# Kernel optimization log

Measured on AMD Instinct MI355X. Metric: run time of the kernel, lower is better.

## Reference

```python
import jax, jax.numpy as jnp
import numpy as np

B, N, D = 16, 2048, 1024


def _linear_params(key, d, scale):
    kw, kb = jax.random.split(key)
    W = jax.random.uniform(kw, (d, d), jnp.float32, -scale, scale)
    b = jax.random.uniform(kb, (d,), jnp.float32, -scale, scale)
    return W, b


def setup_inputs() -> dict:
    key = jax.random.key(0)
    ks = jax.random.split(key, 9)
    scale = 1.0 / np.sqrt(D)  # torch nn.Linear default init range
    x1 = jax.random.normal(ks[0], (B, N, D), jnp.float32)
    x2 = jax.random.normal(ks[1], (B, N, D), jnp.float32)
    Wq, bq = _linear_params(ks[2], D, scale)
    Wk, bk = _linear_params(ks[3], D, scale)
    Wv, bv = _linear_params(ks[4], D, scale)
    W1, b1 = _linear_params(ks[5], D, scale)
    W2, b2 = _linear_params(ks[6], D, scale)
    W3, b3 = _linear_params(ks[7], D, scale)
    # torch init is zeros(1); use small nonzero so output/grad paths are exercised
    gamma = jax.random.normal(ks[8], (1,), jnp.float32) * 0.1
    return {"x1": x1, "x2": x2, "Wq": Wq, "bq": bq, "Wk": Wk, "bk": bk,
            "Wv": Wv, "bv": bv, "W1": W1, "b1": b1, "W2": W2, "b2": b2,
            "W3": W3, "b3": b3, "gamma": gamma}


def reference(x1, x2, Wq, bq, Wk, bk, Wv, bv, W1, b1, W2, b2, W3, b3, gamma):
    # QKV cross-attention (unscaled softmax, as in the torch source)
    q = jnp.einsum('bnd,ed->bne', x1, Wq) + bq
    k = jnp.einsum('bnd,ed->bne', x2, Wk) + bk
    v = jnp.einsum('bnd,ed->bne', x2, Wv) + bv
    energy = jnp.einsum('bik,bjk->bij', q, k)          # [B, N, N]
    attn = jax.nn.softmax(energy, axis=-1)
    out = jnp.einsum('bij,bjk->bik', attn, v)          # [B, N, D]
    # multiscale sigmoid gate: sigmoid(s1 + s2 + s3)
    s = (jnp.einsum('bnd,ed->bne', out, W1) + b1
         + jnp.einsum('bnd,ed->bne', out, W2) + b2
         + jnp.einsum('bnd,ed->bne', out, W3) + b3)
    out = out * jax.nn.sigmoid(s)
    return gamma * out + x1
```

## Files before the change

kernel.cpp:

```cpp
#include <hip/hip_runtime.h>
#include <hip/hip_bf16.h>
#include <hip/hip_fp16.h>
#include <cstdint>

#define B_ 16
#define N_ 2048
#define D_ 1024

typedef __attribute__((ext_vector_type(4))) float f32x4;
typedef __attribute__((ext_vector_type(8))) short s16x8;

typedef __attribute__((address_space(1))) const void* gas_ptr;
typedef __attribute__((address_space(3))) void* las_ptr;

__device__ __forceinline__ void gload16(const void* g, void* l)
{
    __builtin_amdgcn_global_load_lds((gas_ptr)(uintptr_t)g, (las_ptr)(uintptr_t)l, 16, 0, 0);
}

__device__ __forceinline__ ushort f2bf(float f)
{
    union { __hip_bfloat16 h; ushort u; } c;
    c.h = __float2bfloat16(f);
    return c.u;
}
__device__ __forceinline__ float bf2f(ushort u)
{
    union { __hip_bfloat16 h; ushort u; } c;
    c.u = u;
    return __bfloat162float(c.h);
}

__global__ __launch_bounds__(256)
void cvt2_bf16(const float* __restrict__ in1, const float* __restrict__ in2,
               ushort* __restrict__ o1, ushort* __restrict__ o2, long n)
{
    long i = ((long)blockIdx.x * 256 + threadIdx.x) * 8;
    const long stride = (long)gridDim.x * 256 * 8;
    for (; i < n; i += stride) {
        f32x4 a = *(const f32x4*)(in1 + i);
        f32x4 b = *(const f32x4*)(in1 + i + 4);
        s16x8 o;
#pragma unroll
        for (int j = 0; j < 4; ++j) { o[j] = (short)f2bf(a[j]); o[4 + j] = (short)f2bf(b[j]); }
        *(s16x8*)(o1 + i) = o;
        f32x4 c = *(const f32x4*)(in2 + i);
        f32x4 d = *(const f32x4*)(in2 + i + 4);
        s16x8 p;
#pragma unroll
        for (int j = 0; j < 4; ++j) { p[j] = (short)f2bf(c[j]); p[4 + j] = (short)f2bf(d[j]); }
        *(s16x8*)(o2 + i) = p;
    }
}

__global__ __launch_bounds__(256)
void prep_w(const float* __restrict__ Wq, const float* __restrict__ Wk, const float* __restrict__ Wv,
            const float* __restrict__ W1, const float* __restrict__ W2, const float* __restrict__ W3,
            const float* __restrict__ b1, const float* __restrict__ b2, const float* __restrict__ b3,
            const float* __restrict__ bq, const float* __restrict__ bk,
            ushort* __restrict__ wq, ushort* __restrict__ wk, ushort* __restrict__ wv,
            ushort* __restrict__ wsum, float* __restrict__ bsum, float* __restrict__ bqk)
{
    const long i = ((long)blockIdx.x * 256 + threadIdx.x) * 4;
    if (i < (long)D_ * D_) {
#pragma unroll
        for (int j = 0; j < 4; ++j) {
            wq[i + j] = f2bf(Wq[i + j]);
            wk[i + j] = f2bf(Wk[i + j]);
            wv[i + j] = f2bf(Wv[i + j]);
            wsum[i + j] = f2bf(W1[i + j] + W2[i + j] + W3[i + j]);
        }
        if (i < D_) {
#pragma unroll
            for (int j = 0; j < 4; ++j) {
                bsum[i + j] = b1[i + j] + b2[i + j] + b3[i + j];
                bqk[i + j] = bq[i + j];
                bqk[D_ + i + j] = bk[i + j];
            }
        }
    }
}

template<int EPI>
__global__ __launch_bounds__(512, 2)
void gemm256(const ushort* __restrict__ A, const ushort* __restrict__ Bw,
             void* __restrict__ Out, const float* __restrict__ bias,
             int Nn, int K, int NT,
             long sA, long sB, long sO, int bstride,
             const ushort* __restrict__ outb, const float* __restrict__ x1r,
             const float* __restrict__ gamma)
{
    __shared__ ushort lds[65536];
    const int tid = threadIdx.x;
    const int l = tid & 63;
    const int w = tid >> 6;
    const int wm = w >> 2, wn = w & 3;
    const int lr = l & 15;
    const int c2x = ((((l >> 4) * 16) ^ ((lr & 8) << 2)) >> 1);

    const int gx = gridDim.x, gy = gridDim.y;
    const int nwg = gx * gy * (int)gridDim.z;
    const int orig = ((int)blockIdx.z * gy + blockIdx.y) * gx + blockIdx.x;
    const int swzb = (orig & 7) * (nwg >> 3) + (orig >> 3);
    const int gxy = gx * gy;
    const int bz = swzb / gxy;
    const int rem = swzb - bz * gxy;
    const int by = rem / gx;
    const int bx = rem - by * gx;
    const int m0 = by * 256, n0 = bx * 256;

    const ushort* Ab = A + (long)bz * sA;
    const ushort* Bb = Bw + (long)bz * sB;

    int srow[2], scol[2];
#pragma unroll
    for (int i = 0; i < 2; ++i) {
        const int L = (i * 512 + tid) * 16;
        const int P = L ^ (((L >> 9) & 1) << 5);
        srow[i] = (P >> 6) & 127;
        scol[i] = ((P >> 13) << 5) | ((P & 63) >> 1);
    }
    const int sdst = w * 512;

    f32x4 acc[8][4];
#pragma unroll
    for (int i = 0; i < 8; ++i)
#pragma unroll
        for (int j = 0; j < 4; ++j) acc[i][j] = f32x4{0.f, 0.f, 0.f, 0.f};
    s16x8 a[4][2], b[2][2][2];

#define STAGEH(pl, t)                                                                     \
    if ((t) < NT) {                                                                       \
        const int rb2 = (t) & 1;                                                          \
        const long kk = (long)(t) << 6;                                                   \
        _Pragma("unroll")                                                                 \
        for (int i = 0; i < 2; ++i) {                                                     \
            if ((pl) < 2)                                                                 \
                gload16(Ab + (long)(m0 + (pl) * 128 + srow[i]) * K + kk + scol[i],        \
                        &lds[rb2 * 16384 + (pl) * 8192 + sdst + i * 4096]);               \
            else                                                                          \
                gload16(Bb + (long)(n0 + ((pl) - 2) * 128 + srow[i]) * K + kk + scol[i],  \
                        &lds[32768 + rb2 * 16384 + ((pl) - 2) * 8192 + sdst + i * 4096]); \
        }                                                                                 \
    }

#define LDA_(qm)                                                                           \
    _Pragma("unroll") for (int mi = 0; mi < 4; ++mi)                                       \
    _Pragma("unroll") for (int ks = 0; ks < 2; ++ks)                                       \
        a[mi][ks] = *(const s16x8*)&lds[rbase_a + ks * 4096 + ((qm) * 64 + mi * 16 + lr) * 32 + c2x];

#define LDB_(qn)                                                                           \
    _Pragma("unroll") for (int ni = 0; ni < 2; ++ni)                                       \
    _Pragma("unroll") for (int ks = 0; ks < 2; ++ks)                                       \
        b[qn][ni][ks] = *(const s16x8*)&lds[rbase_b + ks * 4096 +                          \
            ((wn & 1) * 64 + (qn) * 32 + ni * 16 + lr) * 32 + c2x];

#define MM_(qm, qn)                                                                        \
    __builtin_amdgcn_s_setprio(1);                                                         \
    _Pragma("unroll") for (int mi = 0; mi < 4; ++mi)                                       \
    _Pragma("unroll") for (int ni = 0; ni < 2; ++ni)                                       \
    _Pragma("unroll") for (int ks = 0; ks < 2; ++ks)                                       \
        acc[(qm) * 4 + mi][(qn) * 2 + ni] = __builtin_amdgcn_mfma_f32_16x16x32_bf16(       \
            a[mi][ks], b[qn][ni][ks], acc[(qm) * 4 + mi][(qn) * 2 + ni], 0, 0, 0);         \
    __builtin_amdgcn_s_setprio(0);

#define BARR __builtin_amdgcn_s_barrier()

#define KGROUP(tt, VMSTR) {                                          \
    const int rb = (tt) & 1;                                         \
    const int rbase_a = rb * 16384 + wm * 8192;                      \
    const int rbase_b = 32768 + rb * 16384 + (wn >> 1) * 8192;       \
                                                            \
    LDB_(0); LDA_(0);                                                \
    STAGEH(1, (tt) + 1);                                             \
    BARR; MM_(0, 0); BARR;                                           \
                                                            \
    LDB_(1);                                                         \
    STAGEH(2, (tt) + 1);                                             \
    BARR; MM_(0, 1); BARR;                                           \
                                                            \
    LDA_(1);                                                         \
    STAGEH(3, (tt) + 1);                                             \
    BARR; MM_(1, 0); BARR;                                           \
     \
    MM_(1, 1);                                                       \
    STAGEH(0, (tt) + 2);                                             \
    asm volatile("s_waitcnt " VMSTR ::: "memory");                   \
    BARR; }

    STAGEH(0, 0); STAGEH(1, 0); STAGEH(2, 0); STAGEH(3, 0);
    STAGEH(0, 1);
    asm volatile("s_waitcnt vmcnt(2)" ::: "memory");
    BARR;

    int t = 0;
    for (; t < NT - 2; ++t) KGROUP(t, "vmcnt(2)");
    for (; t < NT; ++t) KGROUP(t, "vmcnt(0)");

#undef KGROUP
#undef STAGEH
#undef LDA_
#undef LDB_
#undef MM_

    float gam = 0.f;
    if (EPI == 3) gam = *gamma;
#pragma unroll
    for (int am = 0; am < 8; ++am) {
#pragma unroll
        for (int an = 0; an < 4; ++an) {
#pragma unroll
            for (int r = 0; r < 4; ++r) {
                const int m = m0 + wm * 128 + am * 16 + (l >> 4) * 4 + r;
                const int n = n0 + wn * 64 + an * 16 + lr;
                const float v = acc[am][an][r];
                const long o = (long)bz * sO + (long)m * Nn + n;
                if (EPI == 0) {
                    ((ushort*)Out)[o] = f2bf(v + bias[bz * bstride + n]);
                } else if (EPI == 1) {
                    union { __half h; ushort u; } c;
                    c.h = __float2half(v);
                    ((ushort*)Out)[o] = c.u;
                } else if (EPI == 2) {
                    ((ushort*)Out)[o] = f2bf(v);
                } else if (EPI == 4) {
                    ((ushort*)Out)[o] = f2bf(v + bias[m]);
                } else {
                    const float s = v + bias[n];
                    const float g = 1.f / (1.f + __expf(-s));
                    const float ov = bf2f(outb[(long)m * Nn + n]);
                    ((float*)Out)[o] = gam * ov * g + x1r[(long)m * Nn + n];
                }
            }
        }
    }
}

__global__ __launch_bounds__(256)
void softmax_inplace(ushort* __restrict__ EA)
{
    const long row = blockIdx.x;
    ushort* p = EA + row * N_;
    const int tid = threadIdx.x;
    const int c0 = tid * 8;
    __shared__ float red[8];

    s16x8 raw = *(const s16x8*)(p + c0);
    float v[8];
    float mx = -3.0e38f;
#pragma unroll
    for (int i = 0; i < 8; ++i) {
        union { ushort u; __half h; } c;
        c.u = (ushort)raw[i];
        v[i] = __half2float(c.h);
        mx = fmaxf(mx, v[i]);
    }
#pragma unroll
    for (int off = 32; off > 0; off >>= 1) mx = fmaxf(mx, __shfl_xor(mx, off));
    if ((tid & 63) == 0) red[tid >> 6] = mx;
    __syncthreads();
    mx = fmaxf(fmaxf(red[0], red[1]), fmaxf(red[2], red[3]));

    float s = 0.f;
#pragma unroll
    for (int i = 0; i < 8; ++i) { v[i] = __expf(v[i] - mx); s += v[i]; }
#pragma unroll
    for (int off = 32; off > 0; off >>= 1) s += __shfl_xor(s, off);
    if ((tid & 63) == 0) red[4 + (tid >> 6)] = s;
    __syncthreads();
    s = (red[4] + red[5]) + (red[6] + red[7]);
    const float inv = 1.f / s;

    s16x8 o;
#pragma unroll
    for (int i = 0; i < 8; ++i) o[i] = (short)f2bf(v[i] * inv);
    *(s16x8*)(p + c0) = o;
}

extern "C" void kernel_launch(void* const* d_in, const int* in_sizes, int n_in,
                              void* d_out, int out_size, void* d_ws, size_t ws_size,
                              hipStream_t stream)
{
    const float* x1 = (const float*)d_in[0];
    const float* x2 = (const float*)d_in[1];
    const float* Wq = (const float*)d_in[2];
    const float* bq = (const float*)d_in[3];
    const float* Wk = (const float*)d_in[4];
    const float* bk = (const float*)d_in[5];
    const float* Wv = (const float*)d_in[6];
    const float* bv = (const float*)d_in[7];
    const float* W1 = (const float*)d_in[8];
    const float* b1 = (const float*)d_in[9];
    const float* W2 = (const float*)d_in[10];
    const float* b2 = (const float*)d_in[11];
    const float* W3 = (const float*)d_in[12];
    const float* b3 = (const float*)d_in[13];
    const float* gamma = (const float*)d_in[14];
    float* out = (float*)d_out;

    char* ws = (char*)d_ws;
    const long SZ_XB = (long)B_ * N_ * D_ * 2;
    ushort* x1b  = (ushort*)(ws);
    ushort* x2b  = (ushort*)(ws + SZ_XB);
    ushort* EA   = (ushort*)(ws);
    ushort* wqb  = (ushort*)(ws + 2 * SZ_XB);
    ushort* wkb  = (ushort*)(ws + 2 * SZ_XB + 1L * 2097152);
    ushort* wvb  = (ushort*)(ws + 2 * SZ_XB + 2L * 2097152);
    ushort* wsb  = (ushort*)(ws + 2 * SZ_XB + 3L * 2097152);
    float*  bsum = (float*) (ws + 2 * SZ_XB + 4L * 2097152);
    float*  bqk  = (float*) (ws + 2 * SZ_XB + 4L * 2097152 + 4096);
    char* base2  = ws + 2 * SZ_XB + 4L * 2097152 + 16384;
    ushort* Qb   = (ushort*)(base2);
    ushort* Kb   = (ushort*)(base2 + SZ_XB);
    ushort* Vtb  = (ushort*)(base2 + 2 * SZ_XB);
    ushort* outb = Kb;

    const long NE = (long)B_ * N_ * D_;

    cvt2_bf16<<<4096, 256, 0, stream>>>(x1, x2, x1b, x2b, NE);
    prep_w<<<1024, 256, 0, stream>>>(Wq, Wk, Wv, W1, W2, W3, b1, b2, b3, bq, bk,
                                     wqb, wkb, wvb, wsb, bsum, bqk);

    gemm256<0><<<dim3(4, 128, 2), 512, 0, stream>>>(x1b, wqb, Qb, bqk,
        D_, D_, 16, NE, (long)D_ * D_, NE, D_, nullptr, nullptr, nullptr);

    gemm256<4><<<dim3(8, 4, 16), 512, 0, stream>>>(wvb, x2b, Vtb, bv,
        N_, D_, 16, 0, (long)N_ * D_, (long)D_ * N_, 0,
        nullptr, nullptr, nullptr);

    gemm256<1><<<dim3(8, 8, 16), 512, 0, stream>>>(Qb, Kb, EA, nullptr,
        N_, D_, 16, (long)N_ * D_, (long)N_ * D_, (long)N_ * N_, 0,
        nullptr, nullptr, nullptr);

    softmax_inplace<<<B_ * N_, 256, 0, stream>>>(EA);

    gemm256<2><<<dim3(4, 8, 16), 512, 0, stream>>>(EA, Vtb, outb, nullptr,
        D_, N_, 32, (long)N_ * N_, (long)D_ * N_, (long)N_ * D_, 0,
        nullptr, nullptr, nullptr);

    gemm256<3><<<dim3(4, 128, 1), 512, 0, stream>>>(outb, wsb, out, bsum,
        D_, D_, 16, 0, 0, 0, 0, outb, x1, gamma);
}
```

Baseline: 730.5 us.

## Replace barrier-interleaved k-loop with ping-pong wave ordering and single barrier

Restructures the GEMM main loop so that even and odd waves run their four MFMA quadrants in opposite orders. All four prefetch stages for the next tile are issued up front, and the three intra-iteration barriers are dropped, leaving one barrier per k-step. Prefetch depth shrinks from a partially two-ahead pipeline to strictly one tile ahead with a full vmcnt(0) wait. The aim is to cut barrier stalls and to stagger LDS and MFMA use across waves, at the cost of less latency hiding for global loads.

```diff
diff --git a/kernel.cpp b/kernel.cpp
--- a/kernel.cpp
+++ b/kernel.cpp
@@ -166,36 +166,39 @@
 
 #define BARR __builtin_amdgcn_s_barrier()
 
-#define KGROUP(tt, VMSTR) {                                          \
+#define KGROUP(tt) {                                                 \
     const int rb = (tt) & 1;                                         \
     const int rbase_a = rb * 16384 + wm * 8192;                      \
     const int rbase_b = 32768 + rb * 16384 + (wn >> 1) * 8192;       \
-                                                            \
-    LDB_(0); LDA_(0);                                                \
-    STAGEH(1, (tt) + 1);                                             \
-    BARR; MM_(0, 0); BARR;                                           \
-                                                            \
-    LDB_(1);                                                         \
-    STAGEH(2, (tt) + 1);                                             \
-    BARR; MM_(0, 1); BARR;                                           \
-                                                            \
-    LDA_(1);                                                         \
-    STAGEH(3, (tt) + 1);                                             \
-    BARR; MM_(1, 0); BARR;                                           \
-     \
-    MM_(1, 1);                                                       \
-    STAGEH(0, (tt) + 2);                                             \
-    asm volatile("s_waitcnt " VMSTR ::: "memory");                   \
+    if ((w & 1) == 0) {                                              \
+        LDB_(0); LDA_(0);                                            \
+        STAGEH(0, (tt) + 1); STAGEH(1, (tt) + 1);                    \
+        STAGEH(2, (tt) + 1); STAGEH(3, (tt) + 1);                    \
+        LDB_(1);                                                     \
+        MM_(0, 0);                                                   \
+        MM_(0, 1);                                                   \
+        LDA_(1);                                                     \
+        MM_(1, 0);                                                   \
+        MM_(1, 1);                                                   \
+    } else {                                                         \
+        LDB_(1); LDA_(1);                                            \
+        STAGEH(0, (tt) + 1); STAGEH(1, (tt) + 1);                    \
+        STAGEH(2, (tt) + 1); STAGEH(3, (tt) + 1);                    \
+        LDB_(0);                                                     \
+        MM_(1, 1);                                                   \
+        MM_(1, 0);                                                   \
+        LDA_(0);                                                     \
+        MM_(0, 1);                                                   \
+        MM_(0, 0);                                                   \
+    }                                                                \
+    asm volatile("s_waitcnt vmcnt(0)" ::: "memory");                 \
     BARR; }
 
     STAGEH(0, 0); STAGEH(1, 0); STAGEH(2, 0); STAGEH(3, 0);
-    STAGEH(0, 1);
-    asm volatile("s_waitcnt vmcnt(2)" ::: "memory");
+    asm volatile("s_waitcnt vmcnt(0)" ::: "memory");
     BARR;
 
-    int t = 0;
-    for (; t < NT - 2; ++t) KGROUP(t, "vmcnt(2)");
-    for (; t < NT; ++t) KGROUP(t, "vmcnt(0)");
+    for (int t = 0; t < NT; ++t) KGROUP(t);
 
 #undef KGROUP
 #undef STAGEH
```

Measured after the change: 749.4 us. 1.03x slower.
